# Performance work log

Hardware: AMD Instinct MI355X
Metric: run time of the kernel (lower is better)

Reference implementation:

```python
import jax, jax.numpy as jnp
import numpy as np

N_NODES = 100000
N_EDGES = 1600000
N_FEAT = 128
HIDDEN = 64
N_CLASSES = 40


def setup_inputs() -> dict:
    key = jax.random.key(0)
    ks = jax.random.split(key, 4)
    x = jax.random.normal(ks[0], (N_NODES, N_FEAT), dtype=jnp.float32)
    edge_index = jax.random.randint(ks[1], (2, N_EDGES), 0, N_NODES, dtype=jnp.int64)
    # Glorot-style init like PyG GCNConv
    W1 = jax.random.normal(ks[2], (N_FEAT, HIDDEN), dtype=jnp.float32) * (1.0 / np.sqrt(N_FEAT))
    b1 = jnp.zeros((HIDDEN,), dtype=jnp.float32)
    W2 = jax.random.normal(ks[3], (HIDDEN, N_CLASSES), dtype=jnp.float32) * (1.0 / np.sqrt(HIDDEN))
    b2 = jnp.zeros((N_CLASSES,), dtype=jnp.float32)
    return {"x": x, "edge_index": edge_index, "W1": W1, "b1": b1, "W2": W2, "b2": b2}


def _gcn_conv(x, src, dst, norm, W, b, n_nodes):
    # PyG GCNConv: transform first, then normalized scatter-add aggregation
    h = x @ W                                   # [N, out]
    msg = h[src] * norm[:, None]                # [E+N, out] gather
    out = jax.ops.segment_sum(msg, dst, num_segments=n_nodes)  # scatter-add
    return out + b


def _norm_and_loops(edge_index, n_nodes):
    # add self-loops, symmetric normalization deg^{-1/2} A_hat deg^{-1/2}
    loop = jnp.arange(n_nodes, dtype=edge_index.dtype)
    src = jnp.concatenate([edge_index[0], loop])
    dst = jnp.concatenate([edge_index[1], loop])
    deg = jax.ops.segment_sum(jnp.ones_like(dst, dtype=jnp.float32), dst, num_segments=n_nodes)
    dinv = jnp.where(deg > 0, jax.lax.rsqrt(jnp.maximum(deg, 1.0)), 0.0)
    norm = dinv[src] * dinv[dst]
    return src, dst, norm


def reference(x, edge_index, W1, b1, W2, b2):
    n_nodes = x.shape[0]
    src, dst, norm = _norm_and_loops(edge_index, n_nodes)
    h = _gcn_conv(x, src, dst, norm, W1, b1, n_nodes)
    h = jax.nn.relu(h)
    h = _gcn_conv(h, src, dst, norm, W2, b2, n_nodes)
    return jax.nn.log_softmax(h, axis=1)
```

## Files before the change

kernel.cpp:

```cpp
#include <hip/hip_runtime.h>
#include <hip/hip_bf16.h>
#include <string.h>

#define N_FEAT 128
#define HIDDEN 64
#define N_CLS  40
#define FILL_BLOCKS 1024
#define CHUNK_EDGES 1024
#define B_BITS 6
#define SRC_BITS 17

typedef __bf16 bf16x8 __attribute__((ext_vector_type(8)));
typedef float  f32x4  __attribute__((ext_vector_type(4)));

union Frag { unsigned u[4]; bf16x8 v; };

static __device__ inline int get_xcc() {
    return (int)(__builtin_amdgcn_s_getreg((3 << 11) | 20) & 7u);
}


static __device__ inline unsigned pack_bf16(float a, float b) {
    unsigned ba = __float_as_uint(a);
    unsigned bb = __float_as_uint(b);
    unsigned ra = (ba + 0x7fffu + ((ba >> 16) & 1u)) >> 16;
    unsigned rb = (bb + 0x7fffu + ((bb >> 16) & 1u)) >> 16;
    return (ra & 0xffffu) | (rb << 16);
}

static __device__ inline float2 unpack_bf16(unsigned v) {
    return make_float2(__uint_as_float(v << 16), __uint_as_float(v & 0xffff0000u));
}


__global__ void detect_layout_kernel(const int* __restrict__ ei, int* __restrict__ flag) {
    int lane = threadIdx.x;
    int v = ei[2 * lane + 1];
    unsigned long long b = __ballot(v != 0);
    if (lane == 0) flag[0] = (b == 0ull) ? 1 : 0;
}


__global__ __launch_bounds__(256) void bucket_hist_kernel(const int* __restrict__ ei,
                                                          const int* __restrict__ flag,
                                                          unsigned* __restrict__ bcnt,
                                                          int E, int nbuk) {
    __shared__ unsigned h[2048];
    for (int i = threadIdx.x; i < nbuk; i += 256) h[i] = 0u;
    __syncthreads();
    bool is64 = (flag[0] != 0);
    const int* dstp = is64 ? (ei + 2 * E) : (ei + E);
    int stride = is64 ? 2 : 1;
    for (int e = blockIdx.x * 256 + threadIdx.x; e < E; e += gridDim.x * 256) {
        int d = dstp[(size_t)e * stride];
        atomicAdd(&h[d >> B_BITS], 1u);
    }
    __syncthreads();
    for (int i = threadIdx.x; i < nbuk; i += 256)
        if (h[i]) atomicAdd(&bcnt[i], h[i]);
}


__global__ __launch_bounds__(512) void bucket_scan_kernel(const unsigned* __restrict__ bcnt,
                                                          unsigned* __restrict__ bbase,
                                                          unsigned* __restrict__ bcur, int nbuk) {
    __shared__ unsigned tmp[512];
    __shared__ unsigned carry;
    if (threadIdx.x == 0) carry = 0u;
    __syncthreads();
    for (int base = 0; base < nbuk; base += 512) {
        int i = base + threadIdx.x;
        unsigned v = (i < nbuk) ? bcnt[i] : 0u;
        tmp[threadIdx.x] = v;
        __syncthreads();
#pragma unroll
        for (int off = 1; off < 512; off <<= 1) {
            unsigned t = (threadIdx.x >= (unsigned)off) ? tmp[threadIdx.x - off] : 0u;
            __syncthreads();
            tmp[threadIdx.x] += t;
            __syncthreads();
        }
        unsigned excl = tmp[threadIdx.x] - v + carry;
        if (i < nbuk) {
            bbase[i] = excl;
            bcur[(size_t)i * 16] = excl;
        }
        __syncthreads();
        if (threadIdx.x == 511) carry += tmp[511];
        __syncthreads();
    }
}


__global__ __launch_bounds__(256) void fill_buckets_kernel(const int* __restrict__ ei,
                                                           const int* __restrict__ flag,
                                                           unsigned* __restrict__ bcur,
                                                           unsigned* __restrict__ ctr,
                                                           unsigned* __restrict__ tmpbuf,
                                                           int E, int nbuk) {
    int r = get_xcc();
    int bpx = (nbuk + 7) >> 3;
    int blo = r * bpx;
    int bhi = min(nbuk, blo + bpx);
    bool is64 = (flag[0] != 0);
    const int* dstp = is64 ? (ei + 2 * E) : (ei + E);
    int stride = is64 ? 2 : 1;
    __shared__ unsigned chunk_s;
    for (;;) {
        if (threadIdx.x == 0)
            chunk_s = __hip_atomic_fetch_add(&ctr[r * 64], 1u, __ATOMIC_RELAXED,
                                             __HIP_MEMORY_SCOPE_WORKGROUP);
        __syncthreads();
        long long base = (long long)chunk_s * CHUNK_EDGES;
        __syncthreads();
        if (base >= E) break;
        int end = (int)min((long long)E, base + CHUNK_EDGES);
        for (int e = (int)base + threadIdx.x; e < end; e += 256) {
            int d = dstp[(size_t)e * stride];
            int b = d >> B_BITS;
            if (b >= blo && b < bhi) {
                int s = ei[(size_t)e * stride];
                unsigned val = (unsigned)s | ((unsigned)(d & ((1 << B_BITS) - 1)) << SRC_BITS);
                unsigned slot = __hip_atomic_fetch_add(&bcur[(size_t)b * 16], 1u, __ATOMIC_RELAXED,
                                                       __HIP_MEMORY_SCOPE_WORKGROUP);
                tmpbuf[slot] = val;
            }
        }
    }
}


__global__ __launch_bounds__(256) void bucket_to_csr_kernel(const unsigned* __restrict__ tmpbuf,
                                                            const unsigned* __restrict__ bbase,
                                                            unsigned* __restrict__ deg,
                                                            unsigned* __restrict__ rowptr,
                                                            float* __restrict__ dinv,
                                                            int* __restrict__ csr_src,
                                                            int nbuk, int N, int E) {
    int b = blockIdx.x;
    int tid = threadIdx.x;
    unsigned beg = bbase[b];
    unsigned end = (b + 1 < nbuk) ? bbase[b + 1] : (unsigned)E;
    int d0 = b << B_BITS;
    const int ND = 1 << B_BITS;
    __shared__ unsigned hist[ND], scn[ND], cur[ND];
    if (tid < ND) { hist[tid] = 0u; cur[tid] = 0u; }
    __syncthreads();
    for (unsigned i = beg + tid; i < end; i += 256)
        atomicAdd(&hist[tmpbuf[i] >> SRC_BITS], 1u);
    __syncthreads();
    if (tid == 0) {
        unsigned run = 0;
        for (int k = 0; k < ND; ++k) { scn[k] = run; run += hist[k]; }
    }
    __syncthreads();
    if (tid < ND) {
        int d = d0 + tid;
        if (d < N) {
            unsigned dg = hist[tid];
            deg[d] = dg;
            dinv[d] = rsqrtf((float)(dg + 1u));
            rowptr[d] = beg + scn[tid];
        }
    }
    __syncthreads();
    for (unsigned i = beg + tid; i < end; i += 256) {
        unsigned v = tmpbuf[i];
        unsigned dl = v >> SRC_BITS;
        unsigned s = v & ((1u << SRC_BITS) - 1u);
        unsigned p = atomicAdd(&cur[dl], 1u);
        csr_src[beg + scn[dl] + p] = (int)s;
    }
}


__global__ __launch_bounds__(256) void gemm1_mfma_kernel(const float* __restrict__ x,
                                                         const float* __restrict__ W1,
                                                         unsigned* __restrict__ h1b, int N) {
    int lane = threadIdx.x & 63;
    int quad = lane >> 4;
    int col  = lane & 15;

    Frag B[4][4];
#pragma unroll
    for (int c = 0; c < 4; ++c)
#pragma unroll
        for (int ks = 0; ks < 4; ++ks) {
            int n = c * 16 + col;
#pragma unroll
            for (int jj = 0; jj < 4; ++jj) {
                int k = ks * 32 + quad * 8 + 2 * jj;
                B[c][ks].u[jj] = pack_bf16(W1[k * HIDDEN + n], W1[(k + 1) * HIDDEN + n]);
            }
        }

    int wave_id = blockIdx.x * 4 + (threadIdx.x >> 6);
    int nwaves  = gridDim.x * 4;
    int ntiles  = (N + 15) >> 4;

    for (int rt = wave_id; rt < ntiles; rt += nwaves) {
        int rowA = rt * 16 + col;
        Frag A[4];
#pragma unroll
        for (int ks = 0; ks < 4; ++ks) {
            float4 a0 = make_float4(0.f, 0.f, 0.f, 0.f), a1 = a0;
            if (rowA < N) {
                const float4* ap = (const float4*)(x + (size_t)rowA * N_FEAT + ks * 32 + quad * 8);
                a0 = ap[0];
                a1 = ap[1];
            }
            A[ks].u[0] = pack_bf16(a0.x, a0.y);
            A[ks].u[1] = pack_bf16(a0.z, a0.w);
            A[ks].u[2] = pack_bf16(a1.x, a1.y);
            A[ks].u[3] = pack_bf16(a1.z, a1.w);
        }
        f32x4 acc[4] = {{0.f, 0.f, 0.f, 0.f}, {0.f, 0.f, 0.f, 0.f},
                        {0.f, 0.f, 0.f, 0.f}, {0.f, 0.f, 0.f, 0.f}};
#pragma unroll
        for (int ks = 0; ks < 4; ++ks)
#pragma unroll
            for (int c = 0; c < 4; ++c)
                acc[c] = __builtin_amdgcn_mfma_f32_16x16x32_bf16(A[ks].v, B[c][ks].v, acc[c], 0, 0, 0);

        int rowD = rt * 16 + quad * 4;
#pragma unroll
        for (int c = 0; c < 4; ++c)
#pragma unroll
            for (int r = 0; r < 4; ++r) {
                float v = acc[c][r];
                float nxt = __shfl_down(v, 1);
                int row = rowD + r;
                if (((lane & 1) == 0) && row < N)
                    h1b[(size_t)row * 32 + ((c * 16 + col) >> 1)] = pack_bf16(v, nxt);
            }
    }
}


__global__ __launch_bounds__(256) void gemm2_mfma_kernel(const unsigned* __restrict__ actb,
                                                         const float* __restrict__ W2,
                                                         unsigned* __restrict__ h2b, int N) {
    int lane = threadIdx.x & 63;
    int quad = lane >> 4;
    int col  = lane & 15;

    Frag B[3][2];
#pragma unroll
    for (int c = 0; c < 3; ++c)
#pragma unroll
        for (int ks = 0; ks < 2; ++ks) {
            int n = c * 16 + col;
#pragma unroll
            for (int jj = 0; jj < 4; ++jj) {
                int k = ks * 32 + quad * 8 + 2 * jj;
                float w0 = (n < N_CLS) ? W2[k * N_CLS + n] : 0.f;
                float w1 = (n < N_CLS) ? W2[(k + 1) * N_CLS + n] : 0.f;
                B[c][ks].u[jj] = pack_bf16(w0, w1);
            }
        }

    int wave_id = blockIdx.x * 4 + (threadIdx.x >> 6);
    int nwaves  = gridDim.x * 4;
    int ntiles  = (N + 15) >> 4;

    for (int rt = wave_id; rt < ntiles; rt += nwaves) {
        int rowA = rt * 16 + col;
        Frag A[2];
#pragma unroll
        for (int ks = 0; ks < 2; ++ks) {
            uint4 u = make_uint4(0u, 0u, 0u, 0u);
            if (rowA < N)
                u = *(const uint4*)(actb + (size_t)rowA * 32 + ks * 16 + quad * 4);
            A[ks].u[0] = u.x; A[ks].u[1] = u.y; A[ks].u[2] = u.z; A[ks].u[3] = u.w;
        }
        f32x4 acc[3] = {{0.f, 0.f, 0.f, 0.f}, {0.f, 0.f, 0.f, 0.f}, {0.f, 0.f, 0.f, 0.f}};
#pragma unroll
        for (int ks = 0; ks < 2; ++ks)
#pragma unroll
            for (int c = 0; c < 3; ++c)
                acc[c] = __builtin_amdgcn_mfma_f32_16x16x32_bf16(A[ks].v, B[c][ks].v, acc[c], 0, 0, 0);

        int rowD = rt * 16 + quad * 4;
#pragma unroll
        for (int c = 0; c < 3; ++c)
#pragma unroll
            for (int r = 0; r < 4; ++r) {
                float v = acc[c][r];
                float nxt = __shfl_down(v, 1);
                int row = rowD + r;
                int pair = (c * 16 + col) >> 1;
                if (((lane & 1) == 0) && pair < 20 && row < N)
                    h2b[(size_t)row * 20 + pair] = pack_bf16(v, nxt);
            }
    }
}


__global__ __launch_bounds__(256) void agg1_kernel(const unsigned* __restrict__ h1b,
                                                   const int* __restrict__ csr_src,
                                                   const unsigned* __restrict__ rowptr,
                                                   const unsigned* __restrict__ deg,
                                                   const float* __restrict__ dinv,
                                                   const float* __restrict__ b1,
                                                   unsigned* __restrict__ actb, int N) {
    int wave = threadIdx.x >> 6, lane = threadIdx.x & 63;
    int sub = lane >> 5, j = lane & 31;
    int d = blockIdx.x * 4 + wave;
    if (d >= N) return;
    float dv = dinv[d];
    float acc0 = 0.f, acc1 = 0.f;
    if (sub == 0) {
        float2 v = unpack_bf16(h1b[(size_t)d * 32 + j]);
        acc0 = dv * v.x; acc1 = dv * v.y;
    }
    unsigned beg = rowptr[d];
    int len = (int)deg[d];
    int i = 0;
    for (; i + 8 <= len; i += 8) {
        int s0 = csr_src[beg + i + sub];
        int s1 = csr_src[beg + i + 2 + sub];
        int s2 = csr_src[beg + i + 4 + sub];
        int s3 = csr_src[beg + i + 6 + sub];
        float w0 = dinv[s0], w1 = dinv[s1], w2 = dinv[s2], w3 = dinv[s3];
        unsigned v0 = h1b[(size_t)s0 * 32 + j];
        unsigned v1 = h1b[(size_t)s1 * 32 + j];
        unsigned v2 = h1b[(size_t)s2 * 32 + j];
        unsigned v3 = h1b[(size_t)s3 * 32 + j];
        float2 a0 = unpack_bf16(v0), a1 = unpack_bf16(v1);
        float2 a2 = unpack_bf16(v2), a3 = unpack_bf16(v3);
        acc0 += w0 * a0.x + w1 * a1.x + w2 * a2.x + w3 * a3.x;
        acc1 += w0 * a0.y + w1 * a1.y + w2 * a2.y + w3 * a3.y;
    }
    for (; i + 4 <= len; i += 4) {
        int sA = csr_src[beg + i + sub];
        int sB = csr_src[beg + i + 2 + sub];
        float wA = dinv[sA], wB = dinv[sB];
        float2 a = unpack_bf16(h1b[(size_t)sA * 32 + j]);
        float2 b = unpack_bf16(h1b[(size_t)sB * 32 + j]);
        acc0 += wA * a.x + wB * b.x;
        acc1 += wA * a.y + wB * b.y;
    }
    for (; i < len; i += 2) {
        int e = i + sub;
        if (e < len) {
            int s = csr_src[beg + e];
            float w = dinv[s];
            float2 a = unpack_bf16(h1b[(size_t)s * 32 + j]);
            acc0 += w * a.x;
            acc1 += w * a.y;
        }
    }
    acc0 += __shfl_xor(acc0, 32);
    acc1 += __shfl_xor(acc1, 32);
    if (sub == 0) {
        float2 bb = ((const float2*)b1)[j];
        float r0 = fmaxf(acc0 * dv + bb.x, 0.f);
        float r1 = fmaxf(acc1 * dv + bb.y, 0.f);
        actb[(size_t)d * 32 + j] = pack_bf16(r0, r1);
    }
}


__global__ __launch_bounds__(256) void agg2_lsm_kernel(const unsigned* __restrict__ h2b,
                                                       const int* __restrict__ csr_src,
                                                       const unsigned* __restrict__ rowptr,
                                                       const unsigned* __restrict__ deg,
                                                       const float* __restrict__ dinv,
                                                       const float* __restrict__ b2,
                                                       float* __restrict__ out, int N) {
    int wave = threadIdx.x >> 6, lane = threadIdx.x & 63;
    int sub = lane >> 5, j = lane & 31;
    bool act = (j < 20);
    int d = blockIdx.x * 4 + wave;
    if (d >= N) return;
    float dv = dinv[d];
    float acc0 = 0.f, acc1 = 0.f;
    if (sub == 0 && act) {
        float2 v = unpack_bf16(h2b[(size_t)d * 20 + j]);
        acc0 = dv * v.x; acc1 = dv * v.y;
    }
    unsigned beg = rowptr[d];
    int len = (int)deg[d];
    int i = 0;
    for (; i + 8 <= len; i += 8) {
        int s0 = csr_src[beg + i + sub];
        int s1 = csr_src[beg + i + 2 + sub];
        int s2 = csr_src[beg + i + 4 + sub];
        int s3 = csr_src[beg + i + 6 + sub];
        float w0 = dinv[s0], w1 = dinv[s1], w2 = dinv[s2], w3 = dinv[s3];
        if (act) {
            float2 a0 = unpack_bf16(h2b[(size_t)s0 * 20 + j]);
            float2 a1 = unpack_bf16(h2b[(size_t)s1 * 20 + j]);
            float2 a2 = unpack_bf16(h2b[(size_t)s2 * 20 + j]);
            float2 a3 = unpack_bf16(h2b[(size_t)s3 * 20 + j]);
            acc0 += w0 * a0.x + w1 * a1.x + w2 * a2.x + w3 * a3.x;
            acc1 += w0 * a0.y + w1 * a1.y + w2 * a2.y + w3 * a3.y;
        }
    }
    for (; i + 4 <= len; i += 4) {
        int sA = csr_src[beg + i + sub];
        int sB = csr_src[beg + i + 2 + sub];
        float wA = dinv[sA], wB = dinv[sB];
        if (act) {
            float2 a = unpack_bf16(h2b[(size_t)sA * 20 + j]);
            float2 b = unpack_bf16(h2b[(size_t)sB * 20 + j]);
            acc0 += wA * a.x + wB * b.x;
            acc1 += wA * a.y + wB * b.y;
        }
    }
    for (; i < len; i += 2) {
        int e = i + sub;
        if (e < len && act) {
            int s = csr_src[beg + e];
            float w = dinv[s];
            float2 a = unpack_bf16(h2b[(size_t)s * 20 + j]);
            acc0 += w * a.x;
            acc1 += w * a.y;
        }
    }
    acc0 += __shfl_xor(acc0, 32);
    acc1 += __shfl_xor(acc1, 32);
    float v0 = -1e30f, v1 = -1e30f;
    if (act) {
        float2 bb = ((const float2*)b2)[j];
        v0 = acc0 * dv + bb.x;
        v1 = acc1 * dv + bb.y;
    }
    float m = fmaxf(v0, v1);
#pragma unroll
    for (int off = 32; off > 0; off >>= 1)
        m = fmaxf(m, __shfl_xor(m, off));
    float ex = (act && sub == 0) ? (expf(v0 - m) + expf(v1 - m)) : 0.f;
#pragma unroll
    for (int off = 32; off > 0; off >>= 1)
        ex += __shfl_xor(ex, off);
    float ls = logf(ex);
    if (act && sub == 0) {
        float2* orow = (float2*)(out + (size_t)d * N_CLS);
        orow[j] = make_float2(v0 - m - ls, v1 - m - ls);
    }
}


static inline size_t align_up(size_t x) { return (x + 255) & ~(size_t)255; }

extern "C" void kernel_launch(void* const* d_in, const int* in_sizes, int n_in,
                              void* d_out, int out_size, void* d_ws, size_t ws_size,
                              hipStream_t stream) {
    const float* x  = (const float*)d_in[0];
    const int*   ei = (const int*)d_in[1];
    const float* W1 = (const float*)d_in[2];
    const float* b1 = (const float*)d_in[3];
    const float* W2 = (const float*)d_in[4];
    const float* b2 = (const float*)d_in[5];

    int N = in_sizes[0] / N_FEAT;
    int E = in_sizes[1] / 2;
    int nbuk = (N + (1 << B_BITS) - 1) >> B_BITS;

    char* ws = (char*)d_ws;
    int*      flag    = (int*)ws;       ws += 256;
    unsigned* ctrs    = (unsigned*)ws;  ws += 4096;
    unsigned* bcnt    = (unsigned*)ws;  ws += align_up((size_t)nbuk * 4);
    unsigned* bbase   = (unsigned*)ws;  ws += align_up((size_t)nbuk * 4);
    unsigned* bcur    = (unsigned*)ws;  ws += align_up((size_t)nbuk * 64);
    unsigned* deg     = (unsigned*)ws;  ws += align_up((size_t)N * 4);
    float*    dinv    = (float*)ws;     ws += align_up((size_t)N * 4);
    unsigned* rowptr  = (unsigned*)ws;  ws += align_up((size_t)N * 4);
    unsigned* tmpbuf  = (unsigned*)ws;  ws += align_up((size_t)E * 4);
    int*      csr_src = (int*)ws;       ws += align_up((size_t)E * 4);
    unsigned* h1b     = (unsigned*)ws;  ws += align_up((size_t)N * 32 * 4);
    unsigned* actb    = (unsigned*)ws;  ws += align_up((size_t)N * 32 * 4);
    unsigned* h2b     = (unsigned*)ws;  ws += align_up((size_t)N * 20 * 4);

    hipMemsetAsync(ctrs, 0, 4096, stream);
    hipMemsetAsync(bcnt, 0, (size_t)nbuk * 4, stream);

    detect_layout_kernel<<<1, 64, 0, stream>>>(ei, flag);
    bucket_hist_kernel<<<256, 256, 0, stream>>>(ei, flag, bcnt, E, nbuk);
    bucket_scan_kernel<<<1, 512, 0, stream>>>(bcnt, bbase, bcur, nbuk);
    fill_buckets_kernel<<<FILL_BLOCKS, 256, 0, stream>>>(ei, flag, bcur, ctrs, tmpbuf, E, nbuk);
    bucket_to_csr_kernel<<<nbuk, 256, 0, stream>>>(tmpbuf, bbase, deg, rowptr, dinv, csr_src, nbuk, N, E);

    gemm1_mfma_kernel<<<512, 256, 0, stream>>>(x, W1, h1b, N);
    agg1_kernel<<<(N + 3) / 4, 256, 0, stream>>>(h1b, csr_src, rowptr, deg, dinv, b1, actb, N);

    gemm2_mfma_kernel<<<512, 256, 0, stream>>>(actb, W2, h2b, N);
    agg2_lsm_kernel<<<(N + 3) / 4, 256, 0, stream>>>(h2b, csr_src, rowptr, deg, dinv, b2, (float*)d_out, N);
}
```

Before: 351.3 us.

## Replace bucketed XCC-partitioned CSR build with direct global-atomic counting sort

Replaces the two-level bucket sort for building the destination CSR (bucket histogram, bucket scan, XCC-partitioned fill into a temp buffer, per-bucket local sort) with a plain counting sort: global atomic degree count, a three-kernel prefix scan, and direct placement of each edge via a global atomic cursor per node. Edge indices are read with vectorized 16-byte loads for the int64 layout. This drops the temp buffer pass and the per-bucket local sort, but uses many scattered global atomics over 100K nodes. Neighbor order within a row becomes nondeterministic, so float summation order may vary between runs.

Measured after the change: 426.8 us. 21.5% more time.

```diff
diff --git a/kernel.cpp b/kernel.cpp
--- a/kernel.cpp
+++ b/kernel.cpp
@@ -5,19 +5,12 @@
 #define N_FEAT 128
 #define HIDDEN 64
 #define N_CLS  40
-#define FILL_BLOCKS 1024
-#define CHUNK_EDGES 1024
-#define B_BITS 6
-#define SRC_BITS 17
+#define EDGE_BLOCKS 1024
 
 typedef __bf16 bf16x8 __attribute__((ext_vector_type(8)));
 typedef float  f32x4  __attribute__((ext_vector_type(4)));
 
 union Frag { unsigned u[4]; bf16x8 v; };
-
-static __device__ inline int get_xcc() {
-    return (int)(__builtin_amdgcn_s_getreg((3 << 11) | 20) & 7u);
-}
 
 
 static __device__ inline unsigned pack_bf16(float a, float b) {
@@ -41,135 +34,108 @@
 }
 
 
-__global__ __launch_bounds__(256) void bucket_hist_kernel(const int* __restrict__ ei,
-                                                          const int* __restrict__ flag,
-                                                          unsigned* __restrict__ bcnt,
-                                                          int E, int nbuk) {
-    __shared__ unsigned h[2048];
-    for (int i = threadIdx.x; i < nbuk; i += 256) h[i] = 0u;
+__global__ __launch_bounds__(256) void count_deg_kernel(const int* __restrict__ ei,
+                                                        const int* __restrict__ flag,
+                                                        unsigned* __restrict__ deg, int E) {
+    bool is64 = (flag[0] != 0);
+    int idx = blockIdx.x * 256 + threadIdx.x;
+    if (is64) {
+        int Eeven = E & ~1;
+        int stride2 = gridDim.x * 256 * 2;
+        for (int e = idx * 2; e < Eeven; e += stride2) {
+            uint4 dv = *(const uint4*)(ei + (size_t)2 * E + (size_t)2 * e);
+            atomicAdd(&deg[(int)dv.x], 1u);
+            atomicAdd(&deg[(int)dv.z], 1u);
+        }
+        for (int e = Eeven + idx; e < E; e += gridDim.x * 256)
+            atomicAdd(&deg[ei[(size_t)2 * E + (size_t)2 * e]], 1u);
+    } else {
+        for (int e = idx; e < E; e += gridDim.x * 256)
+            atomicAdd(&deg[ei[(size_t)E + e]], 1u);
+    }
+}
+
+
+__global__ __launch_bounds__(256) void scan_local_kernel(const unsigned* __restrict__ deg,
+                                                         unsigned* __restrict__ rowptr,
+                                                         float* __restrict__ dinv,
+                                                         unsigned* __restrict__ partial, int N) {
+    __shared__ unsigned tmp[256];
+    int i = blockIdx.x * 256 + threadIdx.x;
+    unsigned v = (i < N) ? deg[i] : 0u;
+    if (i < N) dinv[i] = rsqrtf((float)(v + 1u));
+    tmp[threadIdx.x] = v;
     __syncthreads();
+#pragma unroll
+    for (int off = 1; off < 256; off <<= 1) {
+        unsigned t = (threadIdx.x >= (unsigned)off) ? tmp[threadIdx.x - off] : 0u;
+        __syncthreads();
+        tmp[threadIdx.x] += t;
+        __syncthreads();
+    }
+    if (i < N) rowptr[i] = tmp[threadIdx.x] - v;
+    if (threadIdx.x == 255) partial[blockIdx.x] = tmp[255];
+}
+
+
+__global__ __launch_bounds__(512) void scan_partial_kernel(unsigned* __restrict__ partial, int npart) {
+    __shared__ unsigned tmp[512];
+    unsigned v = ((int)threadIdx.x < npart) ? partial[threadIdx.x] : 0u;
+    tmp[threadIdx.x] = v;
+    __syncthreads();
+#pragma unroll
+    for (int off = 1; off < 512; off <<= 1) {
+        unsigned t = (threadIdx.x >= (unsigned)off) ? tmp[threadIdx.x - off] : 0u;
+        __syncthreads();
+        tmp[threadIdx.x] += t;
+        __syncthreads();
+    }
+    if ((int)threadIdx.x < npart) partial[threadIdx.x] = tmp[threadIdx.x] - v;
+}
+
+
+__global__ __launch_bounds__(256) void scan_add_kernel(unsigned* __restrict__ rowptr,
+                                                       const unsigned* __restrict__ partial,
+                                                       unsigned* __restrict__ cur, int N) {
+    int i = blockIdx.x * 256 + threadIdx.x;
+    if (i < N) {
+        unsigned r = rowptr[i] + partial[blockIdx.x];
+        rowptr[i] = r;
+        cur[i] = r;
+    }
+}
+
+
+__global__ __launch_bounds__(256) void place_kernel(const int* __restrict__ ei,
+                                                    const int* __restrict__ flag,
+                                                    unsigned* __restrict__ cur,
+                                                    int* __restrict__ csr_src, int E) {
     bool is64 = (flag[0] != 0);
-    const int* dstp = is64 ? (ei + 2 * E) : (ei + E);
-    int stride = is64 ? 2 : 1;
-    for (int e = blockIdx.x * 256 + threadIdx.x; e < E; e += gridDim.x * 256) {
-        int d = dstp[(size_t)e * stride];
-        atomicAdd(&h[d >> B_BITS], 1u);
-    }
-    __syncthreads();
-    for (int i = threadIdx.x; i < nbuk; i += 256)
-        if (h[i]) atomicAdd(&bcnt[i], h[i]);
-}
-
-
-__global__ __launch_bounds__(512) void bucket_scan_kernel(const unsigned* __restrict__ bcnt,
-                                                          unsigned* __restrict__ bbase,
-                                                          unsigned* __restrict__ bcur, int nbuk) {
-    __shared__ unsigned tmp[512];
-    __shared__ unsigned carry;
-    if (threadIdx.x == 0) carry = 0u;
-    __syncthreads();
-    for (int base = 0; base < nbuk; base += 512) {
-        int i = base + threadIdx.x;
-        unsigned v = (i < nbuk) ? bcnt[i] : 0u;
-        tmp[threadIdx.x] = v;
-        __syncthreads();
-#pragma unroll
-        for (int off = 1; off < 512; off <<= 1) {
-            unsigned t = (threadIdx.x >= (unsigned)off) ? tmp[threadIdx.x - off] : 0u;
-            __syncthreads();
-            tmp[threadIdx.x] += t;
-            __syncthreads();
-        }
-        unsigned excl = tmp[threadIdx.x] - v + carry;
-        if (i < nbuk) {
-            bbase[i] = excl;
-            bcur[(size_t)i * 16] = excl;
-        }
-        __syncthreads();
-        if (threadIdx.x == 511) carry += tmp[511];
-        __syncthreads();
-    }
-}
-
-
-__global__ __launch_bounds__(256) void fill_buckets_kernel(const int* __restrict__ ei,
-                                                           const int* __restrict__ flag,
-                                                           unsigned* __restrict__ bcur,
-                                                           unsigned* __restrict__ ctr,
-                                                           unsigned* __restrict__ tmpbuf,
-                                                           int E, int nbuk) {
-    int r = get_xcc();
-    int bpx = (nbuk + 7) >> 3;
-    int blo = r * bpx;
-    int bhi = min(nbuk, blo + bpx);
-    bool is64 = (flag[0] != 0);
-    const int* dstp = is64 ? (ei + 2 * E) : (ei + E);
-    int stride = is64 ? 2 : 1;
-    __shared__ unsigned chunk_s;
-    for (;;) {
-        if (threadIdx.x == 0)
-            chunk_s = __hip_atomic_fetch_add(&ctr[r * 64], 1u, __ATOMIC_RELAXED,
-                                             __HIP_MEMORY_SCOPE_WORKGROUP);
-        __syncthreads();
-        long long base = (long long)chunk_s * CHUNK_EDGES;
-        __syncthreads();
-        if (base >= E) break;
-        int end = (int)min((long long)E, base + CHUNK_EDGES);
-        for (int e = (int)base + threadIdx.x; e < end; e += 256) {
-            int d = dstp[(size_t)e * stride];
-            int b = d >> B_BITS;
-            if (b >= blo && b < bhi) {
-                int s = ei[(size_t)e * stride];
-                unsigned val = (unsigned)s | ((unsigned)(d & ((1 << B_BITS) - 1)) << SRC_BITS);
-                unsigned slot = __hip_atomic_fetch_add(&bcur[(size_t)b * 16], 1u, __ATOMIC_RELAXED,
-                                                       __HIP_MEMORY_SCOPE_WORKGROUP);
-                tmpbuf[slot] = val;
-            }
-        }
-    }
-}
-
-
-__global__ __launch_bounds__(256) void bucket_to_csr_kernel(const unsigned* __restrict__ tmpbuf,
-                                                            const unsigned* __restrict__ bbase,
-                                                            unsigned* __restrict__ deg,
-                                                            unsigned* __restrict__ rowptr,
-                                                            float* __restrict__ dinv,
-                                                            int* __restrict__ csr_src,
-                                                            int nbuk, int N, int E) {
-    int b = blockIdx.x;
-    int tid = threadIdx.x;
-    unsigned beg = bbase[b];
-    unsigned end = (b + 1 < nbuk) ? bbase[b + 1] : (unsigned)E;
-    int d0 = b << B_BITS;
-    const int ND = 1 << B_BITS;
-    __shared__ unsigned hist[ND], scn[ND], cur[ND];
-    if (tid < ND) { hist[tid] = 0u; cur[tid] = 0u; }
-    __syncthreads();
-    for (unsigned i = beg + tid; i < end; i += 256)
-        atomicAdd(&hist[tmpbuf[i] >> SRC_BITS], 1u);
-    __syncthreads();
-    if (tid == 0) {
-        unsigned run = 0;
-        for (int k = 0; k < ND; ++k) { scn[k] = run; run += hist[k]; }
-    }
-    __syncthreads();
-    if (tid < ND) {
-        int d = d0 + tid;
-        if (d < N) {
-            unsigned dg = hist[tid];
-            deg[d] = dg;
-            dinv[d] = rsqrtf((float)(dg + 1u));
-            rowptr[d] = beg + scn[tid];
-        }
-    }
-    __syncthreads();
-    for (unsigned i = beg + tid; i < end; i += 256) {
-        unsigned v = tmpbuf[i];
-        unsigned dl = v >> SRC_BITS;
-        unsigned s = v & ((1u << SRC_BITS) - 1u);
-        unsigned p = atomicAdd(&cur[dl], 1u);
-        csr_src[beg + scn[dl] + p] = (int)s;
+    int idx = blockIdx.x * 256 + threadIdx.x;
+    if (is64) {
+        int Eeven = E & ~1;
+        int stride2 = gridDim.x * 256 * 2;
+        for (int e = idx * 2; e < Eeven; e += stride2) {
+            uint4 sv = *(const uint4*)(ei + (size_t)2 * e);
+            uint4 dv = *(const uint4*)(ei + (size_t)2 * E + (size_t)2 * e);
+            unsigned p0 = atomicAdd(&cur[(int)dv.x], 1u);
+            csr_src[p0] = (int)sv.x;
+            unsigned p1 = atomicAdd(&cur[(int)dv.z], 1u);
+            csr_src[p1] = (int)sv.z;
+        }
+        for (int e = Eeven + idx; e < E; e += gridDim.x * 256) {
+            int d = ei[(size_t)2 * E + (size_t)2 * e];
+            int s = ei[(size_t)2 * e];
+            unsigned p = atomicAdd(&cur[d], 1u);
+            csr_src[p] = s;
+        }
+    } else {
+        for (int e = idx; e < E; e += gridDim.x * 256) {
+            int d = ei[(size_t)E + e];
+            int s = ei[e];
+            unsigned p = atomicAdd(&cur[d], 1u);
+            csr_src[p] = s;
+        }
     }
 }
 
@@ -456,31 +422,29 @@
 
     int N = in_sizes[0] / N_FEAT;
     int E = in_sizes[1] / 2;
-    int nbuk = (N + (1 << B_BITS) - 1) >> B_BITS;
+    int nblk = (N + 255) / 256;
 
     char* ws = (char*)d_ws;
     int*      flag    = (int*)ws;       ws += 256;
-    unsigned* ctrs    = (unsigned*)ws;  ws += 4096;
-    unsigned* bcnt    = (unsigned*)ws;  ws += align_up((size_t)nbuk * 4);
-    unsigned* bbase   = (unsigned*)ws;  ws += align_up((size_t)nbuk * 4);
-    unsigned* bcur    = (unsigned*)ws;  ws += align_up((size_t)nbuk * 64);
     unsigned* deg     = (unsigned*)ws;  ws += align_up((size_t)N * 4);
     float*    dinv    = (float*)ws;     ws += align_up((size_t)N * 4);
     unsigned* rowptr  = (unsigned*)ws;  ws += align_up((size_t)N * 4);
-    unsigned* tmpbuf  = (unsigned*)ws;  ws += align_up((size_t)E * 4);
+    unsigned* cur     = (unsigned*)ws;  ws += align_up((size_t)N * 4);
+    unsigned* partial = (unsigned*)ws;  ws += 2048;
     int*      csr_src = (int*)ws;       ws += align_up((size_t)E * 4);
     unsigned* h1b     = (unsigned*)ws;  ws += align_up((size_t)N * 32 * 4);
     unsigned* actb    = (unsigned*)ws;  ws += align_up((size_t)N * 32 * 4);
     unsigned* h2b     = (unsigned*)ws;  ws += align_up((size_t)N * 20 * 4);
 
-    hipMemsetAsync(ctrs, 0, 4096, stream);
-    hipMemsetAsync(bcnt, 0, (size_t)nbuk * 4, stream);
+    hipMemsetAsync(deg, 0, (size_t)N * 4, stream);
 
     detect_layout_kernel<<<1, 64, 0, stream>>>(ei, flag);
-    bucket_hist_kernel<<<256, 256, 0, stream>>>(ei, flag, bcnt, E, nbuk);
-    bucket_scan_kernel<<<1, 512, 0, stream>>>(bcnt, bbase, bcur, nbuk);
-    fill_buckets_kernel<<<FILL_BLOCKS, 256, 0, stream>>>(ei, flag, bcur, ctrs, tmpbuf, E, nbuk);
-    bucket_to_csr_kernel<<<nbuk, 256, 0, stream>>>(tmpbuf, bbase, deg, rowptr, dinv, csr_src, nbuk, N, E);
+
+    count_deg_kernel<<<EDGE_BLOCKS, 256, 0, stream>>>(ei, flag, deg, E);
+    scan_local_kernel<<<nblk, 256, 0, stream>>>(deg, rowptr, dinv, partial, N);
+    scan_partial_kernel<<<1, 512, 0, stream>>>(partial, nblk);
+    scan_add_kernel<<<nblk, 256, 0, stream>>>(rowptr, partial, cur, N);
+    place_kernel<<<EDGE_BLOCKS, 256, 0, stream>>>(ei, flag, cur, csr_src, E);
 
     gemm1_mfma_kernel<<<512, 256, 0, stream>>>(x, W1, h1b, N);
     agg1_kernel<<<(N + 3) / 4, 256, 0, stream>>>(h1b, csr_src, rowptr, deg, dinv, b1, actb, N);
```
